# Kernel optimization log

Measured on AMD Instinct MI355X. Metric: run time of the kernel, lower is better.

The kernel has to match this reference:

```python
import jax, jax.numpy as jnp
import numpy as np
import math

N_EMBD = 768
N_HEAD = 12
EPS = 1e-5


def _layernorm(x, scale, bias):
    mu = jnp.mean(x, axis=-1, keepdims=True)
    var = jnp.mean(jnp.square(x - mu), axis=-1, keepdims=True)
    return (x - mu) * jax.lax.rsqrt(var + EPS) * scale + bias


def _new_gelu(x):
    c = math.sqrt(2.0 / math.pi)
    return 0.5 * x * (1.0 + jnp.tanh(c * (x + 0.044715 * x * x * x)))


def setup_inputs() -> dict:
    key = jax.random.key(0)
    ks = jax.random.split(key, 8)
    C = N_EMBD
    x = jax.random.normal(ks[0], (4, 16, C, 16, 16), dtype=jnp.float32)
    s = 0.02
    return {
        "x": x,
        "ln1_scale": jnp.ones((C,), jnp.float32),
        "ln1_bias": jnp.zeros((C,), jnp.float32),
        "Wqkv": jax.random.normal(ks[1], (C, 3 * C), jnp.float32) * s,
        "bqkv": jnp.zeros((3 * C,), jnp.float32),
        "Wattn_proj": jax.random.normal(ks[2], (C, C), jnp.float32) * s,
        "battn_proj": jnp.zeros((C,), jnp.float32),
        "ln2_scale": jnp.ones((C,), jnp.float32),
        "ln2_bias": jnp.zeros((C,), jnp.float32),
        "Wfc": jax.random.normal(ks[3], (C, 4 * C), jnp.float32) * s,
        "bfc": jnp.zeros((4 * C,), jnp.float32),
        "Wmlp_proj": jax.random.normal(ks[4], (4 * C, C), jnp.float32) * s,
        "bmlp_proj": jnp.zeros((C,), jnp.float32),
    }


def _attention(x, Wqkv, bqkv, Wp, bp):
    # x: [B, T, C]
    B, T, C = x.shape
    D = C // N_HEAD
    qkv = x @ Wqkv + bqkv                      # [B, T, 3C]
    q, k, v = jnp.split(qkv, 3, axis=-1)
    q = q.reshape(B, T, N_HEAD, D)
    k = k.reshape(B, T, N_HEAD, D)
    v = v.reshape(B, T, N_HEAD, D)
    att = jnp.einsum("bthd,bshd->bhts", q, k) * (1.0 / math.sqrt(D))
    att = jax.nn.softmax(att, axis=-1)
    y = jnp.einsum("bhts,bshd->bthd", att, v).reshape(B, T, C)
    return y @ Wp + bp


def reference(x, ln1_scale, ln1_bias, Wqkv, bqkv, Wattn_proj, battn_proj,
              ln2_scale, ln2_bias, Wfc, bfc, Wmlp_proj, bmlp_proj):
    v, b, c, h, w = x.shape
    T = h * w
    # v b c h w -> (v b) (h w) c
    xt = x.transpose(0, 1, 3, 4, 2).reshape(v * b, T, c)
    # NOTE: faithful to original — residual base is ln_1(x)
    x1 = _layernorm(xt, ln1_scale, ln1_bias)
    x2 = x1 + _attention(x1, Wqkv, bqkv, Wattn_proj, battn_proj)
    hdn = _new_gelu(_layernorm(x2, ln2_scale, ln2_bias) @ Wfc + bfc)
    x3 = x2 + hdn @ Wmlp_proj + bmlp_proj
    # (v b) (h w) c -> v b c h w
    return x3.reshape(v, b, h, w, c).transpose(0, 1, 4, 2, 3)
```

## Files before the change

kernel.cpp:

```cpp
#include <hip/hip_runtime.h>

typedef unsigned short u16;
typedef unsigned int   u32;
typedef __attribute__((ext_vector_type(4))) float f32x4;
typedef __attribute__((ext_vector_type(8))) short bf16x8;

#define LDS_GLOAD16(gsrc, ldst) \
  __builtin_amdgcn_global_load_lds((const __attribute__((address_space(1))) void*)(gsrc), \
                                   (__attribute__((address_space(3))) void*)(ldst), 16, 0, 0)

__device__ __forceinline__ u16 f2bf(float f) {
  union { float f; u32 u; } x; x.f = f;
  u32 r = x.u + 0x7fffu + ((x.u >> 16) & 1u);
  return (u16)(r >> 16);
}
__device__ __forceinline__ float bf2f(u16 h) {
  union { u32 u; float f; } x; x.u = ((u32)h) << 16; return x.f;
}
__device__ __forceinline__ float bflo(u32 u) {
  union { u32 u; float f; } x; x.u = u << 16; return x.f;
}
__device__ __forceinline__ float bfhi(u32 u) {
  union { u32 u; float f; } x; x.u = u & 0xffff0000u; return x.f;
}
__device__ __forceinline__ float gelu_f(float x) {
  const float c = 0.7978845608028654f;
  float u = c * (x + 0.044715f * x * x * x);
  float e = __expf(2.0f * u);
  float t = (e - 1.0f) / (e + 1.0f);
  return 0.5f * x * (1.0f + t);
}

__global__ __launch_bounds__(256) void wtrans_kernel(const float* __restrict__ W,
                                                     u16* __restrict__ Wt, int K, int N) {
  int k = blockIdx.x * 256 + threadIdx.x;
  int n = blockIdx.y;
  Wt[(size_t)n * K + k] = f2bf(W[(size_t)k * N + n]);
}

__global__ __launch_bounds__(256) void ln1_partial(const float* __restrict__ x,
    float* __restrict__ p1, float* __restrict__ p2) {
  const int cx = blockIdx.x, vb = blockIdx.y, t = threadIdx.x;
  const float* xp = x + ((size_t)vb * 768 + (size_t)cx * 64) * 256 + t;
  float s1 = 0.f, s2 = 0.f;
#pragma unroll 8
  for (int cc = 0; cc < 64; ++cc) {
    const float v = xp[(size_t)cc * 256];
    s1 += v; s2 += v * v;
  }
  p1[((size_t)vb * 12 + cx) * 256 + t] = s1;
  p2[((size_t)vb * 12 + cx) * 256 + t] = s2;
}

__global__ __launch_bounds__(256) void ln1_stats(const float* __restrict__ p1,
    const float* __restrict__ p2, float* __restrict__ meanv, float* __restrict__ rstdv) {
  const int i = blockIdx.x * 256 + threadIdx.x;
  const int vb = i >> 8, t = i & 255;
  float s1 = 0.f, s2 = 0.f;
#pragma unroll
  for (int cx = 0; cx < 12; ++cx) {
    s1 += p1[((size_t)vb * 12 + cx) * 256 + t];
    s2 += p2[((size_t)vb * 12 + cx) * 256 + t];
  }
  const float mean = s1 * (1.0f / 768.0f);
  const float var = s2 * (1.0f / 768.0f) - mean * mean;
  meanv[i] = mean;
  rstdv[i] = rsqrtf(var + 1e-5f);
}

__global__ __launch_bounds__(256) void ln1_norm(const float* __restrict__ x,
    const float* __restrict__ meanv, const float* __restrict__ rstdv,
    const float* __restrict__ sc, const float* __restrict__ bi, u16* __restrict__ x1) {
  const int cx = blockIdx.x, vb = blockIdx.y, t = threadIdx.x;
  __shared__ u16 tile[64][258];
  const float mean = meanv[vb * 256 + t];
  const float rstd = rstdv[vb * 256 + t];
  const float* xp = x + ((size_t)vb * 768 + (size_t)cx * 64) * 256 + t;
#pragma unroll 8
  for (int cc = 0; cc < 64; ++cc) {
    const int c = cx * 64 + cc;
    const float v = (xp[(size_t)cc * 256] - mean) * rstd * sc[c] + bi[c];
    tile[cc][t] = f2bf(v);
  }
  __syncthreads();
#pragma unroll
  for (int i = 0; i < 8; ++i) {
    const int g = i * 256 + t;
    const int tok = g >> 3, j = g & 7;
    u16 tmp[8];
#pragma unroll
    for (int jj = 0; jj < 8; ++jj) tmp[jj] = tile[j * 8 + jj][tok];
    uint4 o;
    o.x = (u32)tmp[0] | ((u32)tmp[1] << 16);
    o.y = (u32)tmp[2] | ((u32)tmp[3] << 16);
    o.z = (u32)tmp[4] | ((u32)tmp[5] << 16);
    o.w = (u32)tmp[6] | ((u32)tmp[7] << 16);
    *(uint4*)(x1 + (size_t)(vb * 256 + tok) * 768 + cx * 64 + j * 8) = o;
  }
}

__global__ __launch_bounds__(256) void ln2_kernel(const u16* __restrict__ x2,
    const float* __restrict__ sc, const float* __restrict__ bi, u16* __restrict__ out) {
  const int row = blockIdx.x, tid = threadIdx.x;
  const u16* xp = x2 + (size_t)row * 768;
  const float v0 = bf2f(xp[tid]);
  const float v1 = bf2f(xp[tid + 256]);
  const float v2 = bf2f(xp[tid + 512]);
  float s1 = v0 + v1 + v2;
  float s2 = v0 * v0 + v1 * v1 + v2 * v2;
#pragma unroll
  for (int m = 1; m < 64; m <<= 1) { s1 += __shfl_xor(s1, m); s2 += __shfl_xor(s2, m); }
  __shared__ float w1[4], w2[4];
  if ((tid & 63) == 0) { w1[tid >> 6] = s1; w2[tid >> 6] = s2; }
  __syncthreads();
  s1 = w1[0] + w1[1] + w1[2] + w1[3];
  s2 = w2[0] + w2[1] + w2[2] + w2[3];
  const float mean = s1 * (1.0f / 768.0f);
  const float var = s2 * (1.0f / 768.0f) - mean * mean;
  const float rstd = rsqrtf(var + 1e-5f);
  u16* op = out + (size_t)row * 768;
  op[tid]       = f2bf((v0 - mean) * rstd * sc[tid]       + bi[tid]);
  op[tid + 256] = f2bf((v1 - mean) * rstd * sc[tid + 256] + bi[tid + 256]);
  op[tid + 512] = f2bf((v2 - mean) * rstd * sc[tid + 512] + bi[tid + 512]);
}

template<int EPI>
__global__ __launch_bounds__(256) void gemm_bt(
    const u16* __restrict__ A, const u16* __restrict__ Bt,
    const float* __restrict__ bias, const u16* __restrict__ resid,
    void* __restrict__ outp, int M, int N, int K)
{
  __shared__ u16 As[128 * 32];
  __shared__ u16 Bs[128 * 32];
  const int tid = threadIdx.x;
  const int lane = tid & 63;
  const int wave = tid >> 6;
  const int wr = wave >> 1, wc = wave & 1;
  const int m0 = blockIdx.y * 128;
  const int n0 = blockIdx.x * 128;

  const u16* a0 = A + (size_t)(m0 + (tid >> 2)) * K + (tid & 3) * 8;
  const u16* a1 = a0 + (size_t)64 * K;
  const u16* b0 = Bt + (size_t)(n0 + (tid >> 2)) * K + (tid & 3) * 8;
  const u16* b1 = b0 + (size_t)64 * K;
  u16* asd0 = As + tid * 8;        u16* asd1 = As + 2048 + tid * 8;
  u16* bsd0 = Bs + tid * 8;        u16* bsd1 = Bs + 2048 + tid * 8;

  f32x4 acc[4][4] = {};

  for (int kt = 0; kt < K; kt += 32) {
    LDS_GLOAD16(a0, asd0);
    LDS_GLOAD16(a1, asd1);
    LDS_GLOAD16(b0, bsd0);
    LDS_GLOAD16(b1, bsd1);
    a0 += 32; a1 += 32; b0 += 32; b1 += 32;
    __syncthreads();
    bf16x8 af[4], bfr[4];
#pragma unroll
    for (int i = 0; i < 4; ++i) {
      af[i]  = *(const bf16x8*)(As + (wr * 64 + i * 16 + (lane & 15)) * 32 + (lane >> 4) * 8);
      bfr[i] = *(const bf16x8*)(Bs + (wc * 64 + i * 16 + (lane & 15)) * 32 + (lane >> 4) * 8);
    }
#pragma unroll
    for (int i = 0; i < 4; ++i)
#pragma unroll
      for (int j = 0; j < 4; ++j)
        acc[i][j] = __builtin_amdgcn_mfma_f32_16x16x32_bf16(af[i], bfr[j], acc[i][j], 0, 0, 0);
    __syncthreads();
  }

  const int colb = n0 + wc * 64 + (lane & 15);
  const int rowb = m0 + wr * 64 + ((lane >> 4) << 2);
#pragma unroll
  for (int i = 0; i < 4; ++i) {
#pragma unroll
    for (int j = 0; j < 4; ++j) {
      const int c = colb + j * 16;
      const float bv = bias[c];
      if (EPI == 3) {
        const int r0 = rowb + i * 16;
        const int vb = r0 >> 8, t = r0 & 255;
        float vals[4];
#pragma unroll
        for (int q = 0; q < 4; ++q) {
          const int r = r0 + q;
          vals[q] = acc[i][j][q] + bv + bf2f(resid[(size_t)r * N + c]);
        }
        float4 o; o.x = vals[0]; o.y = vals[1]; o.z = vals[2]; o.w = vals[3];
        *(float4*)((float*)outp + ((size_t)vb * 768 + c) * 256 + t) = o;
      } else {
#pragma unroll
        for (int q = 0; q < 4; ++q) {
          const int r = rowb + i * 16 + q;
          float v = acc[i][j][q] + bv;
          if (EPI == 1) v += bf2f(resid[(size_t)r * N + c]);
          if (EPI == 2) v = gelu_f(v);
          ((u16*)outp)[(size_t)r * N + c] = f2bf(v);
        }
      }
    }
  }
}

__global__ __launch_bounds__(256, 1) void attn_mfma(const u16* __restrict__ qkv,
                                                    u16* __restrict__ ybuf) {
  __shared__ u16 Klds[256 * 64];
  __shared__ u16 Vt[64 * 256];
  __shared__ u16 Plds[4][64 * 64];
  const int tid = threadIdx.x;
  const int lane = tid & 63;
  const int wave = tid >> 6;
  const int bh = blockIdx.x;
  const int b = bh / 12, h = bh % 12;
  const size_t base = (size_t)b * 256 * 2304 + (size_t)h * 64;

#pragma unroll
  for (int it = 0; it < 8; ++it) {
    const int g = it * 256 + tid;
    const int tok = g >> 3, s = g & 7;
    const int oct = s ^ (tok & 7);
    LDS_GLOAD16(qkv + base + (size_t)tok * 2304 + 768 + oct * 8, Klds + (size_t)g * 8);
  }

  bf16x8 qf[4][2];
#pragma unroll
  for (int i = 0; i < 4; ++i) {
    const int r = wave * 64 + i * 16 + (lane & 15);
    const u16* qp = qkv + base + (size_t)r * 2304 + (lane >> 4) * 8;
    qf[i][0] = *(const bf16x8*)qp;
    qf[i][1] = *(const bf16x8*)(qp + 32);
  }

  uint4 vld[8];
#pragma unroll
  for (int o = 0; o < 8; ++o)
    vld[o] = *(const uint4*)(qkv + base + (size_t)tid * 2304 + 1536 + o * 8);
#pragma unroll
  for (int o = 0; o < 8; ++o) {
    const u32 w[4] = {vld[o].x, vld[o].y, vld[o].z, vld[o].w};
#pragma unroll
    for (int j = 0; j < 8; ++j) {
      const int d = o * 8 + j;
      const int byteoff = (d * 512 + tid * 2) ^ ((d & 7) << 4);
      *(u16*)((char*)Vt + byteoff) = (u16)(w[j >> 1] >> ((j & 1) * 16));
    }
  }
  __syncthreads();

  u16* Pw = Plds[wave];
  f32x4 ya[4][4] = {};
  float lrow[4][4] = {};

  for (int c = 0; c < 4; ++c) {
    const int tc0 = c * 64;
    f32x4 sa[4][4] = {};
#pragma unroll
    for (int kt = 0; kt < 2; ++kt) {
      bf16x8 kf[4];
#pragma unroll
      for (int jj = 0; jj < 4; ++jj) {
        const int tok = tc0 + jj * 16 + (lane & 15);
        const int bo = (tok * 128 + kt * 64 + (lane >> 4) * 16) ^ ((tok & 7) << 4);
        kf[jj] = *(const bf16x8*)((const char*)Klds + bo);
      }
#pragma unroll
      for (int i = 0; i < 4; ++i)
#pragma unroll
        for (int jj = 0; jj < 4; ++jj)
          sa[i][jj] = __builtin_amdgcn_mfma_f32_16x16x32_bf16(qf[i][kt], kf[jj], sa[i][jj], 0, 0, 0);
    }
#pragma unroll
    for (int i = 0; i < 4; ++i) {
#pragma unroll
      for (int q = 0; q < 4; ++q) {
        const int prow = i * 16 + (lane >> 4) * 4 + q;
        float psum = 0.f;
#pragma unroll
        for (int jj = 0; jj < 4; ++jj) {
          const float p = __expf(sa[i][jj][q] * 0.125f);
          psum += p;
          const int pcol = jj * 16 + (lane & 15);
          const int pb = (prow * 128 + pcol * 2) ^ ((prow & 7) << 4);
          *(u16*)((char*)Pw + pb) = f2bf(p);
        }
        lrow[i][q] += psum;
      }
    }
#pragma unroll
    for (int kt2 = 0; kt2 < 2; ++kt2) {
      bf16x8 pf[4], vf[4];
#pragma unroll
      for (int i = 0; i < 4; ++i) {
        const int qrow = i * 16 + (lane & 15);
        const int pb = (qrow * 128 + kt2 * 64 + (lane >> 4) * 16) ^ ((qrow & 7) << 4);
        pf[i] = *(const bf16x8*)((const char*)Pw + pb);
      }
#pragma unroll
      for (int j = 0; j < 4; ++j) {
        const int dd = j * 16 + (lane & 15);
        const int vb_ = (dd * 512 + (tc0 + kt2 * 32) * 2 + (lane >> 4) * 16) ^ ((dd & 7) << 4);
        vf[j] = *(const bf16x8*)((const char*)Vt + vb_);
      }
#pragma unroll
      for (int i = 0; i < 4; ++i)
#pragma unroll
        for (int j = 0; j < 4; ++j)
          ya[i][j] = __builtin_amdgcn_mfma_f32_16x16x32_bf16(pf[i], vf[j], ya[i][j], 0, 0, 0);
    }
  }

  float linv[4][4];
#pragma unroll
  for (int i = 0; i < 4; ++i)
#pragma unroll
    for (int q = 0; q < 4; ++q) {
      float s = lrow[i][q];
      s += __shfl_xor(s, 1); s += __shfl_xor(s, 2);
      s += __shfl_xor(s, 4); s += __shfl_xor(s, 8);
      linv[i][q] = 1.0f / s;
    }
#pragma unroll
  for (int i = 0; i < 4; ++i) {
    const int row0 = wave * 64 + i * 16 + ((lane >> 4) << 2);
#pragma unroll
    for (int j = 0; j < 4; ++j) {
      const int dd = j * 16 + (lane & 15);
#pragma unroll
      for (int q = 0; q < 4; ++q)
        ybuf[(size_t)(b * 256 + row0 + q) * 768 + h * 64 + dd] = f2bf(ya[i][j][q] * linv[i][q]);
    }
  }
}

extern "C" void kernel_launch(void* const* d_in, const int* in_sizes, int n_in,
                              void* d_out, int out_size, void* d_ws, size_t ws_size,
                              hipStream_t stream) {
  (void)in_sizes; (void)n_in; (void)out_size; (void)ws_size;
  const float* x    = (const float*)d_in[0];
  const float* ln1s = (const float*)d_in[1];
  const float* ln1b = (const float*)d_in[2];
  const float* Wqkv = (const float*)d_in[3];
  const float* bqkv = (const float*)d_in[4];
  const float* Wap  = (const float*)d_in[5];
  const float* bap  = (const float*)d_in[6];
  const float* ln2s = (const float*)d_in[7];
  const float* ln2b = (const float*)d_in[8];
  const float* Wfc  = (const float*)d_in[9];
  const float* bfc  = (const float*)d_in[10];
  const float* Wmlp = (const float*)d_in[11];
  const float* bmlp = (const float*)d_in[12];

  char* ws = (char*)d_ws;
  u16* WqkvT = (u16*)(ws + 0);
  u16* WpT   = (u16*)(ws + 3538944);
  u16* WfcT  = (u16*)(ws + 4718592);
  u16* WmlpT = (u16*)(ws + 9437184);
  u16* x1    = (u16*)(ws + 14155776);
  u16* x2    = (u16*)(ws + 39321600);
  u16* qkv   = (u16*)(ws + 64487424);
  u16* ybuf  = (u16*)(ws + 139984896);
  u16* hbuf  = (u16*)(ws + 64487424);
  float* p1    = (float*)(ws + 165150720);
  float* p2    = (float*)(ws + 165937152);
  float* meanv = (float*)(ws + 166723584);
  float* rstdv = (float*)(ws + 166789120);
  u16* x2n = x1;

  wtrans_kernel<<<dim3(3, 2304), 256, 0, stream>>>(Wqkv, WqkvT, 768, 2304);
  wtrans_kernel<<<dim3(3, 768),  256, 0, stream>>>(Wap,  WpT,   768, 768);
  wtrans_kernel<<<dim3(3, 3072), 256, 0, stream>>>(Wfc,  WfcT,  768, 3072);
  wtrans_kernel<<<dim3(12, 768), 256, 0, stream>>>(Wmlp, WmlpT, 3072, 768);

  ln1_partial<<<dim3(12, 64), 256, 0, stream>>>(x, p1, p2);
  ln1_stats<<<64, 256, 0, stream>>>(p1, p2, meanv, rstdv);
  ln1_norm<<<dim3(12, 64), 256, 0, stream>>>(x, meanv, rstdv, ln1s, ln1b, x1);

  gemm_bt<0><<<dim3(18, 128), 256, 0, stream>>>(x1, WqkvT, bqkv, nullptr, qkv, 16384, 2304, 768);

  attn_mfma<<<768, 256, 0, stream>>>(qkv, ybuf);

  gemm_bt<1><<<dim3(6, 128), 256, 0, stream>>>(ybuf, WpT, bap, x1, x2, 16384, 768, 768);

  ln2_kernel<<<16384, 256, 0, stream>>>(x2, ln2s, ln2b, x2n);

  gemm_bt<2><<<dim3(24, 128), 256, 0, stream>>>(x2n, WfcT, bfc, nullptr, hbuf, 16384, 3072, 768);

  gemm_bt<3><<<dim3(6, 128), 256, 0, stream>>>(hbuf, WmlpT, bmlp, x2, (float*)d_out, 16384, 768, 3072);
}
```

Measured before the change: 689.6 us.

## Triple-buffer GEMM LDS staging with XOR swizzle and grouped block remap

```diff
diff --git a/kernel.cpp b/kernel.cpp
--- a/kernel.cpp
+++ b/kernel.cpp
@@ -124,49 +124,73 @@
   op[tid + 512] = f2bf((v2 - mean) * rstd * sc[tid + 512] + bi[tid + 512]);
 }
 
+#define STAGE_GEMM(dstbase) do { \
+  LDS_GLOAD16(a0, (u16*)(dstbase) + tid * 8); \
+  LDS_GLOAD16(a1, (u16*)(dstbase) + 2048 + tid * 8); \
+  LDS_GLOAD16(b0, (u16*)(dstbase) + 4096 + tid * 8); \
+  LDS_GLOAD16(b1, (u16*)(dstbase) + 6144 + tid * 8); \
+  a0 += 32; a1 += 32; b0 += 32; b1 += 32; \
+} while (0)
+
 template<int EPI>
 __global__ __launch_bounds__(256) void gemm_bt(
     const u16* __restrict__ A, const u16* __restrict__ Bt,
     const float* __restrict__ bias, const u16* __restrict__ resid,
     void* __restrict__ outp, int M, int N, int K)
 {
-  __shared__ u16 As[128 * 32];
-  __shared__ u16 Bs[128 * 32];
+  __shared__ u16 Sm[3][8192];
   const int tid = threadIdx.x;
   const int lane = tid & 63;
   const int wave = tid >> 6;
   const int wr = wave >> 1, wc = wave & 1;
-  const int m0 = blockIdx.y * 128;
-  const int n0 = blockIdx.x * 128;
-
-  const u16* a0 = A + (size_t)(m0 + (tid >> 2)) * K + (tid & 3) * 8;
+
+  const int nxg = gridDim.x;
+  const int nwg = nxg * gridDim.y;
+  const int orig = blockIdx.y * nxg + blockIdx.x;
+  const int qch = nwg >> 3;
+  const int wg = (orig & 7) * qch + (orig >> 3);
+  const int n0 = (wg % nxg) * 128;
+  const int m0 = (wg / nxg) * 128;
+
+  const int srow = tid >> 2;
+  const int oct = (tid & 3) ^ ((tid >> 3) & 3);
+  const u16* a0 = A + (size_t)(m0 + srow) * K + oct * 8;
   const u16* a1 = a0 + (size_t)64 * K;
-  const u16* b0 = Bt + (size_t)(n0 + (tid >> 2)) * K + (tid & 3) * 8;
+  const u16* b0 = Bt + (size_t)(n0 + srow) * K + oct * 8;
   const u16* b1 = b0 + (size_t)64 * K;
-  u16* asd0 = As + tid * 8;        u16* asd1 = As + 2048 + tid * 8;
-  u16* bsd0 = Bs + tid * 8;        u16* bsd1 = Bs + 2048 + tid * 8;
 
   f32x4 acc[4][4] = {};
-
-  for (int kt = 0; kt < K; kt += 32) {
-    LDS_GLOAD16(a0, asd0);
-    LDS_GLOAD16(a1, asd1);
-    LDS_GLOAD16(b0, bsd0);
-    LDS_GLOAD16(b1, bsd1);
-    a0 += 32; a1 += 32; b0 += 32; b1 += 32;
-    __syncthreads();
+  const int nt = K >> 5;
+
+  STAGE_GEMM((char*)Sm);
+  if (nt > 1) STAGE_GEMM((char*)Sm + 16384);
+
+  int curb = 0, preb = 32768;
+  for (int t = 0; t < nt; ++t) {
+    asm volatile("s_waitcnt lgkmcnt(0)" ::: "memory");
+    if (t < nt - 1) { asm volatile("s_waitcnt vmcnt(4)" ::: "memory"); }
+    else            { asm volatile("s_waitcnt vmcnt(0)" ::: "memory"); }
+    __builtin_amdgcn_s_barrier();
+    asm volatile("" ::: "memory");
+    if (t + 2 < nt) STAGE_GEMM((char*)Sm + preb);
+
+    const char* smc = (const char*)Sm + curb;
     bf16x8 af[4], bfr[4];
 #pragma unroll
     for (int i = 0; i < 4; ++i) {
-      af[i]  = *(const bf16x8*)(As + (wr * 64 + i * 16 + (lane & 15)) * 32 + (lane >> 4) * 8);
-      bfr[i] = *(const bf16x8*)(Bs + (wc * 64 + i * 16 + (lane & 15)) * 32 + (lane >> 4) * 8);
+      const int ar = wr * 64 + i * 16 + (lane & 15);
+      af[i]  = *(const bf16x8*)(smc + ar * 64 + (((lane >> 4) ^ ((ar >> 1) & 3)) << 4));
+      const int br = wc * 64 + i * 16 + (lane & 15);
+      bfr[i] = *(const bf16x8*)(smc + 8192 + br * 64 + (((lane >> 4) ^ ((br >> 1) & 3)) << 4));
     }
 #pragma unroll
     for (int i = 0; i < 4; ++i)
 #pragma unroll
       for (int j = 0; j < 4; ++j)
         acc[i][j] = __builtin_amdgcn_mfma_f32_16x16x32_bf16(af[i], bfr[j], acc[i][j], 0, 0, 0);
-    __syncthreads();
+
+    curb += 16384; if (curb == 49152) curb = 0;
+    preb += 16384; if (preb == 49152) preb = 0;
   }
 
   const int colb = n0 + wc * 64 + (lane & 15);
```

After: 569.4 us. -17.4%, faster.
